# Optimization experiments

Hardware: AMD Instinct MI355X
Metric: run time of the kernel (lower is better)

## Reference

```python
import jax, jax.numpy as jnp
import numpy as np

N_BINS = 15


def _ece(logits, labels):
    # logits: [N, C] float, labels: [N] int
    probs = jax.nn.softmax(logits, axis=1)
    confidences = jnp.max(probs, axis=1)                      # [N]
    predictions = jnp.argmax(probs, axis=1)                   # [N]
    accuracies = (predictions == labels).astype(jnp.float32)  # [N]

    # bin i covers (lowers[i], lowers[i]+1/n_bins]; matches gt(lower)*le(upper)
    lowers = jnp.linspace(0.0, 1.0, N_BINS + 1)[:-1]          # [n_bins]
    bin_idx = jnp.sum(confidences[:, None] > lowers[None, :], axis=1) - 1  # [N]
    valid = (bin_idx >= 0).astype(jnp.float32)
    bin_idx = jnp.clip(bin_idx, 0, N_BINS - 1)

    n = confidences.shape[0]
    cnt = jax.ops.segment_sum(valid, bin_idx, num_segments=N_BINS)
    conf_sum = jax.ops.segment_sum(confidences * valid, bin_idx, num_segments=N_BINS)
    acc_sum = jax.ops.segment_sum(accuracies * valid, bin_idx, num_segments=N_BINS)

    prop_in_bin = cnt / n
    safe_cnt = jnp.maximum(cnt, 1.0)
    avg_conf = conf_sum / safe_cnt
    avg_acc = acc_sum / safe_cnt
    nonempty = cnt > 0

    ece = jnp.sum(jnp.where(nonempty, jnp.abs(avg_conf - avg_acc) * prop_in_bin, 0.0))
    acc = jnp.sum(jnp.where(nonempty, avg_acc * prop_in_bin, 0.0))
    return jnp.reshape(ece * 100.0, (1,)), jnp.reshape(acc * 100.0, (1,))


def setup_inputs() -> dict:
    key = jax.random.key(0)
    k1, k2 = jax.random.split(key)
    N, C = 65536, 1000
    logits = jax.random.normal(k1, (N, C), dtype=jnp.float32)
    labels = jax.random.randint(k2, (N,), 0, C, dtype=jnp.int64)
    return {"logits": logits, "labels": labels}


def reference(logits, labels):
    return _ece(logits, labels)
```

## Files before the change

### kernel.cpp

```cpp
#include <hip/hip_runtime.h>
#include <hip/hip_bf16.h>
#include <math.h>

#define NBINS 15
#define NB1 2048
#define BLK 256

__global__ __launch_bounds__(BLK, 4) void ece_rows_kernel(
    const float* __restrict__ logits,
    const int*   __restrict__ labels,
    float* __restrict__ partials,
    int N, int C)
{
    __shared__ float sb[3 * NBINS];

    const int t = threadIdx.x;
    if (t < 3 * NBINS) sb[t] = 0.0f;
    __syncthreads();

    const int lane   = t & 63;
    const int wave   = (blockIdx.x * BLK + t) >> 6;
    const int nwaves = (NB1 * BLK) >> 6;
    const int nvec   = (C + 3) >> 2;

    for (int row = wave; row < N; row += nwaves) {
        const float4* __restrict__ rp = (const float4*)(logits + (size_t)row * C);

        float4 v[4];
        #pragma unroll
        for (int k = 0; k < 4; ++k) {
            int idx = lane + 64 * k;
            v[k] = (idx < nvec) ? rp[idx]
                                : make_float4(-INFINITY, -INFINITY, -INFINITY, -INFINITY);
        }

        float s0 = 0.f, s1 = 0.f, s2 = 0.f, s3 = 0.f;
        float m = -INFINITY;
        int   am = 0;
        #pragma unroll
        for (int k = 0; k < 4; ++k) {
            const float* e = (const float*)&v[k];
            int col = (lane + 64 * k) * 4;
            s0 += __expf(e[0]);
            s1 += __expf(e[1]);
            s2 += __expf(e[2]);
            s3 += __expf(e[3]);
            #pragma unroll
            for (int j = 0; j < 4; ++j) {
                float x = e[j];
                if (x > m) { m = x; am = col + j; }
            }
        }
        float s = (s0 + s1) + (s2 + s3);

        #pragma unroll
        for (int off = 32; off; off >>= 1) {
            float m2  = __shfl_xor(m,  off, 64);
            float sv  = __shfl_xor(s,  off, 64);
            int   am2 = __shfl_xor(am, off, 64);
            s += sv;
            if (m2 > m || (m2 == m && am2 < am)) { m = m2; am = am2; }
        }

        if (lane == 0) {
            float conf = __expf(m) / s;
            float acc  = (am == labels[row]) ? 1.0f : 0.0f;
            int b = 0;
            #pragma unroll
            for (int k = 1; k < NBINS; ++k)
                b += (conf > (float)k * (1.0f / 15.0f)) ? 1 : 0;
            atomicAdd(&sb[b],             1.0f);
            atomicAdd(&sb[NBINS + b],     conf);
            atomicAdd(&sb[2 * NBINS + b], acc);
        }
    }

    __syncthreads();
    if (t < 3 * NBINS)
        partials[(size_t)t * NB1 + blockIdx.x] = sb[t];
}

__global__ __launch_bounds__(1024) void ece_final_kernel(
    const float* __restrict__ partials, float* __restrict__ out, int N)
{
    __shared__ double red[3 * NBINS][16];
    const int t = threadIdx.x;
    const int c = t >> 4;
    const int sub = t & 15;

    if (c < 3 * NBINS) {
        double a = 0.0;
        for (int b = sub; b < NB1; b += 16)
            a += (double)partials[(size_t)c * NB1 + b];
        red[c][sub] = a;
    }
    __syncthreads();
    if (t < 3 * NBINS) {
        double ssum = 0.0;
        #pragma unroll
        for (int i = 0; i < 16; ++i) ssum += red[t][i];
        red[t][0] = ssum;
    }
    __syncthreads();
    if (t == 0) {
        double ece = 0.0, acc = 0.0;
        const double n = (double)N;
        for (int k = 0; k < NBINS; ++k) {
            double cnt = red[k][0];
            double cs  = red[NBINS + k][0];
            double as  = red[2 * NBINS + k][0];
            if (cnt > 0.0) {
                double avg_conf = cs / cnt;
                double avg_acc  = as / cnt;
                double prop     = cnt / n;
                ece += fabs(avg_conf - avg_acc) * prop;
                acc += avg_acc * prop;
            }
        }
        out[0] = (float)(ece * 100.0);
        out[1] = (float)(acc * 100.0);
    }
}

extern "C" void kernel_launch(void* const* d_in, const int* in_sizes, int n_in,
                              void* d_out, int out_size, void* d_ws, size_t ws_size,
                              hipStream_t stream) {
    const float* logits = (const float*)d_in[0];
    const int*   labels = (const int*)d_in[1];
    float* out = (float*)d_out;

    const int N = in_sizes[1];
    const int C = in_sizes[0] / N;

    float* partials = (float*)d_ws;

    ece_rows_kernel<<<NB1, BLK, 0, stream>>>(logits, labels, partials, N, C);
    ece_final_kernel<<<1, 1024, 0, stream>>>(partials, out, N);
}
```

Before: 385.8 us.

## Prefetch next row into registers and pack argmax into 64-bit shuffle key

Software-pipelines the per-wave row loop so the next row's logits and label are loaded into registers while the current row is reduced, hiding global memory latency. It also replaces the sequential compare-and-update argmax with a branchless max and equality scan. The max and its index are packed into one sortable 64-bit key, so the wave reduction does a single compare per step. The cost is doubled register pressure for the row buffers, which could lower occupancy under the launch bounds.

```diff
diff --git a/kernel.cpp b/kernel.cpp
--- a/kernel.cpp
+++ b/kernel.cpp
@@ -13,7 +13,6 @@
     int N, int C)
 {
     __shared__ float sb[3 * NBINS];
-
     const int t = threadIdx.x;
     if (t < 3 * NBINS) sb[t] = 0.0f;
     __syncthreads();
@@ -23,48 +22,84 @@
     const int nwaves = (NB1 * BLK) >> 6;
     const int nvec   = (C + 3) >> 2;
 
-    for (int row = wave; row < N; row += nwaves) {
+    const int  i0 = lane, i1 = lane + 64, i2 = lane + 128, i3 = lane + 192;
+    const bool q0 = i0 < nvec, q1 = i1 < nvec, q2 = i2 < nvec, q3 = i3 < nvec;
+    const float4 NEG = make_float4(-INFINITY, -INFINITY, -INFINITY, -INFINITY);
+
+    float4 v0 = NEG, v1 = NEG, v2 = NEG, v3 = NEG;
+    int lab = 0;
+    int row = wave;
+    if (row < N) {
         const float4* __restrict__ rp = (const float4*)(logits + (size_t)row * C);
+        v0 = q0 ? rp[i0] : NEG;
+        v1 = q1 ? rp[i1] : NEG;
+        v2 = q2 ? rp[i2] : NEG;
+        v3 = q3 ? rp[i3] : NEG;
+        lab = labels[row];
+    }
 
-        float4 v[4];
-        #pragma unroll
-        for (int k = 0; k < 4; ++k) {
-            int idx = lane + 64 * k;
-            v[k] = (idx < nvec) ? rp[idx]
-                                : make_float4(-INFINITY, -INFINITY, -INFINITY, -INFINITY);
+    while (row < N) {
+        const int nrow = row + nwaves;
+        float4 w0 = NEG, w1 = NEG, w2 = NEG, w3 = NEG;
+        int nlab = 0;
+        if (nrow < N) {
+            const float4* __restrict__ rp = (const float4*)(logits + (size_t)nrow * C);
+            w0 = q0 ? rp[i0] : NEG;
+            w1 = q1 ? rp[i1] : NEG;
+            w2 = q2 ? rp[i2] : NEG;
+            w3 = q3 ? rp[i3] : NEG;
+            nlab = labels[nrow];
         }
 
-        float s0 = 0.f, s1 = 0.f, s2 = 0.f, s3 = 0.f;
-        float m = -INFINITY;
-        int   am = 0;
-        #pragma unroll
-        for (int k = 0; k < 4; ++k) {
-            const float* e = (const float*)&v[k];
-            int col = (lane + 64 * k) * 4;
-            s0 += __expf(e[0]);
-            s1 += __expf(e[1]);
-            s2 += __expf(e[2]);
-            s3 += __expf(e[3]);
+        const float* e0 = (const float*)&v0;
+        const float* e1 = (const float*)&v1;
+        const float* e2 = (const float*)&v2;
+        const float* e3 = (const float*)&v3;
+
+        float s0 = __expf(e0[0]) + __expf(e0[1]) + __expf(e0[2]) + __expf(e0[3]);
+        float s1 = __expf(e1[0]) + __expf(e1[1]) + __expf(e1[2]) + __expf(e1[3]);
+        float s2 = __expf(e2[0]) + __expf(e2[1]) + __expf(e2[2]) + __expf(e2[3]);
+        float s3 = __expf(e3[0]) + __expf(e3[1]) + __expf(e3[2]) + __expf(e3[3]);
+        float s  = (s0 + s1) + (s2 + s3);
+
+        float m0 = fmaxf(fmaxf(e0[0], e0[1]), fmaxf(e0[2], e0[3]));
+        float m1 = fmaxf(fmaxf(e1[0], e1[1]), fmaxf(e1[2], e1[3]));
+        float m2 = fmaxf(fmaxf(e2[0], e2[1]), fmaxf(e2[2], e2[3]));
+        float m3 = fmaxf(fmaxf(e3[0], e3[1]), fmaxf(e3[2], e3[3]));
+        float m  = fmaxf(fmaxf(m0, m1), fmaxf(m2, m3));
+
+        int am = 0x7FFFFFFF;
+        {
+            const float* es[4] = { e0, e1, e2, e3 };
             #pragma unroll
-            for (int j = 0; j < 4; ++j) {
-                float x = e[j];
-                if (x > m) { m = x; am = col + j; }
+            for (int k = 3; k >= 0; --k) {
+                const int base = (lane + 64 * k) * 4;
+                #pragma unroll
+                for (int j = 3; j >= 0; --j)
+                    am = (es[k][j] == m) ? (base + j) : am;
             }
         }
-        float s = (s0 + s1) + (s2 + s3);
+
+        unsigned int mb = __float_as_uint(m);
+        unsigned int ms = mb ^ ((unsigned int)((int)mb >> 31) | 0x80000000u);
+        unsigned long long key =
+            ((unsigned long long)ms << 32) | (unsigned int)(0x7FFFFFFF - am);
 
         #pragma unroll
         for (int off = 32; off; off >>= 1) {
-            float m2  = __shfl_xor(m,  off, 64);
-            float sv  = __shfl_xor(s,  off, 64);
-            int   am2 = __shfl_xor(am, off, 64);
+            unsigned long long k2 = __shfl_xor(key, off, 64);
+            float sv              = __shfl_xor(s,   off, 64);
             s += sv;
-            if (m2 > m || (m2 == m && am2 < am)) { m = m2; am = am2; }
+            key = (k2 > key) ? k2 : key;
         }
 
         if (lane == 0) {
-            float conf = __expf(m) / s;
-            float acc  = (am == labels[row]) ? 1.0f : 0.0f;
+            unsigned int msr = (unsigned int)(key >> 32);
+            unsigned int mbr = (msr & 0x80000000u) ? (msr ^ 0x80000000u) : ~msr;
+            float mw   = __uint_as_float(mbr);
+            int   amw  = 0x7FFFFFFF - (int)(unsigned int)(key & 0xFFFFFFFFu);
+            float conf = __expf(mw) / s;
+            float acc  = (amw == lab) ? 1.0f : 0.0f;
             int b = 0;
             #pragma unroll
             for (int k = 1; k < NBINS; ++k)
@@ -73,6 +108,9 @@
             atomicAdd(&sb[NBINS + b],     conf);
             atomicAdd(&sb[2 * NBINS + b], acc);
         }
+
+        row = nrow;
+        v0 = w0; v1 = w1; v2 = w2; v3 = w3; lab = nlab;
     }
 
     __syncthreads();
```

Measured after the change: 389.3 us. About the same (+0.9%).
